# Performance work log

Measured on AMD Instinct MI355X. Metric: run time of the kernel, lower is better.

The kernel has to match this reference:

```python
import jax, jax.numpy as jnp
import numpy as np

ALPHA = 0.3

def setup_inputs() -> dict:
    key = jax.random.key(0)
    k1, k2, k3, k4 = jax.random.split(key, 4)
    bz, sl, n_pos = 64, 1024, 50
    a_arc = jax.random.normal(k1, (bz, sl, sl), dtype=jnp.float32)
    s_arc = jax.random.normal(k2, (bz, sl, sl), dtype=jnp.float32)
    adds = jax.random.randint(k3, (bz, sl), 0, n_pos, dtype=jnp.int32)
    pos = jax.random.randint(k4, (bz, sl), 0, n_pos, dtype=jnp.int32)
    return {"a_arc": a_arc, "s_arc": s_arc, "adds": adds, "pos": pos, "n_pos": n_pos}


def reference(a_arc, s_arc, adds, pos, n_pos):
    # Bin index for every (head, dep) pair: bin = adds[b,i]*n_pos + adds[b,j]
    bins_add = adds[:, :, None] * n_pos + adds[:, None, :]          # [bz, sl, sl] int32
    # Histogram: sum a_arc values per POS-pair bin (replaces the O(n_pos^2) masked loop)
    score_arc = jax.ops.segment_sum(
        a_arc.reshape(-1), bins_add.reshape(-1), num_segments=n_pos * n_pos)
    score_arc = jax.nn.sigmoid(score_arc)                            # [n_pos^2]
    # Broadcast the binned scores back onto s_arc via the pos-pair bins
    bins_pos = pos[:, :, None] * n_pos + pos[:, None, :]             # [bz, sl, sl]
    return s_arc + ALPHA * score_arc[bins_pos]
```

## Files before the change

### kernel.cpp

```cpp
#include <hip/hip_runtime.h>

constexpr int NPOS  = 50;
constexpr int NBINS = NPOS * NPOS;
constexpr int SL    = 1024;
constexpr int BZ    = 64;
constexpr float ALPHA = 0.3f;

using nat_f4 = __attribute__((ext_vector_type(4))) float;

constexpr int NRNG      = 8;
constexpr int PSLICE    = 352;
constexpr int H_THREADS = 256;
constexpr int H_BLOCKS  = BZ * NRNG;

__device__ __forceinline__ int rng_lo(int r) { return r < 2 ? 7 * r : 14 + 6 * (r - 2); }
__device__ __forceinline__ int rng_sz(int r) { return r < 2 ? 7 : 6; }

constexpr int R2_THREADS = 256;
constexpr int R2_BLOCKS  = (NBINS + R2_THREADS - 1) / R2_THREADS;
constexpr int A_THREADS      = 256;
constexpr int ROWS_PER_BLOCK = 32;
constexpr int BLOCKS_PER_B   = SL / ROWS_PER_BLOCK;
constexpr int A_BLOCKS       = BZ * BLOCKS_PER_B;

__global__ __launch_bounds__(H_THREADS) void hist_gather(
    const float* __restrict__ a, const int* __restrict__ adds,
    float* __restrict__ g_part) {
  __shared__ int   adds_s[SL];
  __shared__ float accL[8][SL];
  __shared__ int   list[SL + 8];
  __shared__ int   order2[SL];
  __shared__ int   cnt8[8], off8[8];
  __shared__ int   cntQ[NPOS], offQs[NPOS], offQm[NPOS];
  __shared__ int   nrows_s;

  const int tid = threadIdx.x;
  const int b   = blockIdx.x / NRNG;
  const int rg  = blockIdx.x % NRNG;
  const int lo  = rng_lo(rg), sz = rng_sz(rg);

  ((int4*)adds_s)[tid] = ((const int4*)(adds + (size_t)b * SL))[tid];
  #pragma unroll
  for (int p = 0; p < 8; ++p) ((float4*)&accL[p][0])[tid] = float4{0, 0, 0, 0};
  if (tid < 8) cnt8[tid] = 0;
  if (tid < NPOS) cntQ[tid] = 0;
  __syncthreads();

  for (int i = tid; i < SL; i += H_THREADS) {
    const int p = adds_s[i];
    const int pl = p - lo;
    if ((unsigned)pl < (unsigned)sz) atomicAdd(&cnt8[pl], 1);
    atomicAdd(&cntQ[p], 1);
  }
  __syncthreads();
  if (tid == 0) {
    int run = 0;
    #pragma unroll
    for (int c = 0; c < 8; ++c) { off8[c] = run; run += cnt8[c]; }
    nrows_s = run;
  } else if (tid == 64) {
    int run = 0;
    for (int c = 0; c < NPOS; ++c) { offQs[c] = run; offQm[c] = run; run += cntQ[c]; }
  }
  __syncthreads();
  for (int i = tid; i < SL; i += H_THREADS) {
    const int p = adds_s[i];
    const int pl = p - lo;
    if ((unsigned)pl < (unsigned)sz)
      list[atomicAdd(&off8[pl], 1)] = (pl << 12) | i;
    order2[atomicAdd(&offQm[p], 1)] = i;
  }
  __syncthreads();
  const int N    = nrows_s;
  const int Npad = (N + 7) & ~7;
  if (tid < 8 && N + tid < Npad)
    list[N + tid] = (7 << 12) | (N > 0 ? (list[N - 1] & 0xFFF) : 0);
  __syncthreads();

  const nat_f4* __restrict__ Ab = (const nat_f4*)(a + (size_t)b * SL * SL);
  float4 creg = {0, 0, 0, 0};
  int pcur = 7;

  int    eA[8], eB[8];
  nat_f4 vA[8], vB[8];
  auto loadbank = [&](int (&e)[8], nat_f4 (&v)[8], int k) {
    #pragma unroll
    for (int u = 0; u < 8; ++u) {
      e[u] = __builtin_amdgcn_readfirstlane(list[k + u]);
      v[u] = __builtin_nontemporal_load(
          Ab + (size_t)(e[u] & 0xFFF) * (SL / 4) + tid);
    }
  };
  auto procbank = [&](int (&e)[8], nat_f4 (&v)[8]) {
    #pragma unroll
    for (int u = 0; u < 8; ++u) {
      const int pl = e[u] >> 12;
      if (pl != pcur) {
        ((float4*)&accL[pcur][0])[tid] = creg;
        creg = float4{0, 0, 0, 0};
        pcur = pl;
      }
      creg.x += v[u][0]; creg.y += v[u][1]; creg.z += v[u][2]; creg.w += v[u][3];
    }
  };

  if (Npad > 0) {
    pcur = list[0] >> 12;
    loadbank(eA, vA, 0);
    for (int k = 0; k < Npad; k += 16) {
      if (k + 8 < Npad) loadbank(eB, vB, k + 8);
      procbank(eA, vA);
      if (k + 16 < Npad) loadbank(eA, vA, k + 16);
      if (k + 8 < Npad) procbank(eB, vB);
    }
    ((float4*)&accL[pcur][0])[tid] = creg;
  }
  __syncthreads();

  float* __restrict__ gp = g_part + (size_t)blockIdx.x * PSLICE;
  for (int bin = tid; bin < sz * NPOS; bin += H_THREADS) {
    const int pl = bin / NPOS, q = bin % NPOS;
    const int s0 = offQs[q], n = cntQ[q];
    float s = 0.0f;
    for (int k2 = 0; k2 < n; ++k2) s += accL[pl][order2[s0 + k2]];
    gp[bin] = s;
  }
}

__global__ __launch_bounds__(R2_THREADS) void reduce2(
    const float* __restrict__ g_part, float* __restrict__ g_hist) {
  const int bin = blockIdx.x * R2_THREADS + threadIdx.x;
  if (bin >= NBINS) return;
  const int p = bin / NPOS, q = bin % NPOS;
  const int rg = (p < 14) ? p / 7 : 2 + (p - 14) / 6;
  const int pl = (p < 14) ? p % 7 : (p - 14) % 6;
  float s = 0.0f;
  #pragma unroll 8
  for (int bb = 0; bb < BZ; ++bb)
    s += g_part[(size_t)(bb * NRNG + rg) * PSLICE + pl * NPOS + q];
  g_hist[bin] = s;
}

__global__ __launch_bounds__(A_THREADS) void apply_kernel(
    const float* __restrict__ s, const int* __restrict__ pos,
    const float* __restrict__ g_hist, float* __restrict__ out) {
  __shared__ float sig[NBINS];
  __shared__ int   pos_s[SL];

  const int tid = threadIdx.x;
  const int b   = blockIdx.x / BLOCKS_PER_B;
  const int i0  = (blockIdx.x % BLOCKS_PER_B) * ROWS_PER_BLOCK;

  ((int4*)pos_s)[tid] = ((const int4*)(pos + (size_t)b * SL))[tid];
  for (int k = tid; k < NBINS; k += A_THREADS) {
    const float h = g_hist[k];
    sig[k] = 1.0f / (1.0f + __expf(-h));
  }
  __syncthreads();

  const int4 pj = ((const int4*)pos_s)[tid];
  const size_t rowoff = ((size_t)b * SL + i0) * SL;
  const nat_f4* __restrict__ srow = (const nat_f4*)(s + rowoff);
  nat_f4* __restrict__ orow = (nat_f4*)(out + rowoff);

  for (int r = 0; r < ROWS_PER_BLOCK; ++r) {
    const int base = pos_s[i0 + r] * NPOS;
    const nat_f4 sv =
        __builtin_nontemporal_load(srow + (size_t)r * (SL / 4) + tid);
    nat_f4 ov;
    ov[0] = sv[0] + ALPHA * sig[base + pj.x];
    ov[1] = sv[1] + ALPHA * sig[base + pj.y];
    ov[2] = sv[2] + ALPHA * sig[base + pj.z];
    ov[3] = sv[3] + ALPHA * sig[base + pj.w];
    __builtin_nontemporal_store(ov, orow + (size_t)r * (SL / 4) + tid);
  }
}

extern "C" void kernel_launch(void* const* d_in, const int* in_sizes, int n_in,
                              void* d_out, int out_size, void* d_ws, size_t ws_size,
                              hipStream_t stream) {
  const float* a_arc = (const float*)d_in[0];
  const float* s_arc = (const float*)d_in[1];
  const int*   adds  = (const int*)d_in[2];
  const int*   pos   = (const int*)d_in[3];
  float* out    = (float*)d_out;
  float* g_hist = (float*)d_ws;
  float* g_part = g_hist + 4096;

  hist_gather <<<H_BLOCKS, H_THREADS, 0, stream>>>(a_arc, adds, g_part);
  reduce2     <<<R2_BLOCKS, R2_THREADS, 0, stream>>>(g_part, g_hist);
  apply_kernel<<<A_BLOCKS, A_THREADS, 0, stream>>>(s_arc, pos, g_hist, out);
}
```

Measured before the change: 155.3 us.

## Split histogram gather blocks into row halves to double block count

Each histogram block now handles only half of the rows for its POS range, doubling the grid of hist_gather blocks to improve occupancy and latency hiding on the a_arc stream. The per-q ordering tables are still built over all rows in every block, and each half writes its own partial slice, which reduce2 now sums pairwise. This adds duplicated setup and finalisation work per block and doubles partial-sum traffic.

```diff
diff --git a/kernel.cpp b/kernel.cpp
--- a/kernel.cpp
+++ b/kernel.cpp
@@ -9,9 +9,10 @@
 using nat_f4 = __attribute__((ext_vector_type(4))) float;
 
 constexpr int NRNG      = 8;
+constexpr int NHALF     = 2;
 constexpr int PSLICE    = 352;
 constexpr int H_THREADS = 256;
-constexpr int H_BLOCKS  = BZ * NRNG;
+constexpr int H_BLOCKS  = BZ * NRNG * NHALF;
 
 __device__ __forceinline__ int rng_lo(int r) { return r < 2 ? 7 * r : 14 + 6 * (r - 2); }
 __device__ __forceinline__ int rng_sz(int r) { return r < 2 ? 7 : 6; }
@@ -28,16 +29,19 @@
     float* __restrict__ g_part) {
   __shared__ int   adds_s[SL];
   __shared__ float accL[8][SL];
-  __shared__ int   list[SL + 8];
+  __shared__ int   list[512 + 8];
   __shared__ int   order2[SL];
   __shared__ int   cnt8[8], off8[8];
   __shared__ int   cntQ[NPOS], offQs[NPOS], offQm[NPOS];
   __shared__ int   nrows_s;
 
-  const int tid = threadIdx.x;
-  const int b   = blockIdx.x / NRNG;
-  const int rg  = blockIdx.x % NRNG;
-  const int lo  = rng_lo(rg), sz = rng_sz(rg);
+  const int tid  = threadIdx.x;
+  const int b    = blockIdx.x / (NRNG * NHALF);
+  const int rem  = blockIdx.x % (NRNG * NHALF);
+  const int rg   = rem >> 1;
+  const int half = rem & 1;
+  const int lo   = rng_lo(rg), sz = rng_sz(rg);
+  const int rlo  = half * (SL / NHALF), rhi = rlo + SL / NHALF;
 
   ((int4*)adds_s)[tid] = ((const int4*)(adds + (size_t)b * SL))[tid];
   #pragma unroll
@@ -46,11 +50,10 @@
   if (tid < NPOS) cntQ[tid] = 0;
   __syncthreads();
 
-  for (int i = tid; i < SL; i += H_THREADS) {
-    const int p = adds_s[i];
-    const int pl = p - lo;
+  for (int i = tid; i < SL; i += H_THREADS) atomicAdd(&cntQ[adds_s[i]], 1);
+  for (int i = rlo + tid; i < rhi; i += H_THREADS) {
+    const int pl = adds_s[i] - lo;
     if ((unsigned)pl < (unsigned)sz) atomicAdd(&cnt8[pl], 1);
-    atomicAdd(&cntQ[p], 1);
   }
   __syncthreads();
   if (tid == 0) {
@@ -63,13 +66,13 @@
     for (int c = 0; c < NPOS; ++c) { offQs[c] = run; offQm[c] = run; run += cntQ[c]; }
   }
   __syncthreads();
-  for (int i = tid; i < SL; i += H_THREADS) {
-    const int p = adds_s[i];
-    const int pl = p - lo;
+  for (int i = rlo + tid; i < rhi; i += H_THREADS) {
+    const int pl = adds_s[i] - lo;
     if ((unsigned)pl < (unsigned)sz)
       list[atomicAdd(&off8[pl], 1)] = (pl << 12) | i;
-    order2[atomicAdd(&offQm[p], 1)] = i;
-  }
+  }
+  for (int i = tid; i < SL; i += H_THREADS)
+    order2[atomicAdd(&offQm[adds_s[i]], 1)] = i;
   __syncthreads();
   const int N    = nrows_s;
   const int Npad = (N + 7) & ~7;
@@ -134,10 +137,14 @@
   const int p = bin / NPOS, q = bin % NPOS;
   const int rg = (p < 14) ? p / 7 : 2 + (p - 14) / 6;
   const int pl = (p < 14) ? p % 7 : (p - 14) % 6;
+  const float* __restrict__ base =
+      g_part + (size_t)(rg * NHALF) * PSLICE + pl * NPOS + q;
   float s = 0.0f;
   #pragma unroll 8
-  for (int bb = 0; bb < BZ; ++bb)
-    s += g_part[(size_t)(bb * NRNG + rg) * PSLICE + pl * NPOS + q];
+  for (int bb = 0; bb < BZ; ++bb) {
+    const size_t o = (size_t)bb * (NRNG * NHALF) * PSLICE;
+    s += base[o] + base[o + PSLICE];
+  }
   g_hist[bin] = s;
 }
 
```

Measured after the change: 159.5 us. +2.7%, slower.
